# Kernel tuning notes

Measured on AMD Instinct MI355X. Metric: run time of the kernel, lower is better.

The kernel has to match this reference:

```python
import jax, jax.numpy as jnp
import numpy as np

B, S, E, H = 4, 2048, 1024, 16
D = E // H  # key_size


def setup_inputs() -> dict:
    key = jax.random.key(0)
    ks = jax.random.split(key, 6)
    s = 1.0 / np.sqrt(E)
    return {
        "X": jax.random.normal(ks[0], (B, S, E), dtype=jnp.float32),
        "Wq": jax.random.uniform(ks[1], (E, E), jnp.float32, -s, s),
        "Wk": jax.random.uniform(ks[2], (E, E), jnp.float32, -s, s),
        "Wv": jax.random.uniform(ks[3], (E, E), jnp.float32, -s, s),
        "Wo": jax.random.uniform(ks[4], (E, E), jnp.float32, -s, s),
        "bo": jax.random.uniform(ks[5], (E,), jnp.float32, -s, s),
    }


def reference(X, Wq, Wk, Wv, Wo, bo):
    # Linear layers: y = x @ W^T (torch convention), no bias for q/k/v
    def split(x):  # [B,S,E] -> [B,H,S,D]
        return x.reshape(B, S, H, D).transpose(0, 2, 1, 3)

    q = split(X @ Wq.T)
    k = split(X @ Wk.T)
    v = split(X @ Wv.T)
    scale = jnp.asarray(np.sqrt(D), dtype=X.dtype)
    scores = jnp.einsum("bhqd,bhkd->bhqk", q, k) / scale
    probs = jax.nn.softmax(scores, axis=-1)
    ctx = jnp.einsum("bhqk,bhkd->bhqd", probs, v)
    out = ctx.transpose(0, 2, 1, 3).reshape(B, S, E)
    return out @ Wo.T + bo
```

## Files before the change

### kernel.cpp

```cpp
#include <hip/hip_runtime.h>
#include <hip/hip_bf16.h>

typedef short bf16x8 __attribute__((ext_vector_type(8)));
typedef float f32x4  __attribute__((ext_vector_type(4)));

__device__ __forceinline__ short f2bf(float f) {
    union { float f; unsigned u; } x; x.f = f;
    unsigned r = x.u + 0x7fffu + ((x.u >> 16) & 1u);
    return (short)(r >> 16);
}

__device__ __forceinline__ unsigned rbits(float f) {
    union { float f; unsigned u; } x; x.f = f;
    return x.u + 0x8000u;
}
__device__ __forceinline__ int pack2(float a, float b) {
    return (int)__builtin_amdgcn_perm(rbits(b), rbits(a), 0x07060302u);
}

__device__ __forceinline__ f32x4 mfma32k(bf16x8 a, bf16x8 b, f32x4 c) {
    return __builtin_amdgcn_mfma_f32_16x16x32_bf16(a, b, c, 0, 0, 0);
}

#define GLDS16(g, l)                                                            \
    __builtin_amdgcn_global_load_lds(                                           \
        (const __attribute__((address_space(1))) void*)(g),                     \
        (__attribute__((address_space(3))) void*)(l), 16, 0, 0)

static constexpr int Bb = 4, Ss = 2048, Ee = 1024, Hh = 16, Dd = 64;
static constexpr int Mrows = Bb * Ss;
static constexpr float CL2 = 0.1803368801111204f;

__global__ void cvt_all(const float* __restrict__ X,  const float* __restrict__ Wq,
                        const float* __restrict__ Wk, const float* __restrict__ Wv,
                        const float* __restrict__ Wo,
                        short* __restrict__ Xb, short* __restrict__ Wqk,
                        short* __restrict__ Wvb, short* __restrict__ Wob) {
    int bid = blockIdx.x;
    const float* src; short* dst; int off; float scale = 1.0f;
    if (bid < 8192) {
        src = X; dst = Xb; off = bid * 1024;
    } else {
        int wsel = (bid - 8192) >> 10;
        off = ((bid - 8192) & 1023) * 1024;
        if      (wsel == 0) { src = Wq; dst = Wqk;                scale = CL2; }
        else if (wsel == 1) { src = Wk; dst = Wqk + Ee * Ee; }
        else if (wsel == 2) { src = Wv; dst = Wvb; }
        else                { src = Wo; dst = Wob; }
    }
    int i = off + threadIdx.x * 4;
    float4 v = *(const float4*)(src + i);
    short4 o;
    o.x = f2bf(v.x * scale); o.y = f2bf(v.y * scale);
    o.z = f2bf(v.z * scale); o.w = f2bf(v.w * scale);
    *(short4*)(dst + i) = o;
}

__global__ __launch_bounds__(256, 2)
void gemm_fused(const short* __restrict__ A0, const short* __restrict__ B0,
                short* __restrict__ C0,
                const short* __restrict__ A1, const short* __restrict__ B1,
                short* __restrict__ C1, int split) {
    __shared__ __align__(16) short sA[128 * 32];
    __shared__ __align__(16) short sB[128 * 32];
    const int t = threadIdx.x, w = t >> 6, l = t & 63;
    const int lane16 = l & 15, quad = l >> 4;
    const int wm = (w >> 1) * 64, wn = (w & 1) * 64;

    int bid = blockIdx.x;
    const short *A, *Bm; short* C;
    int bm, bn, ldc; bool perm;
    if (bid < split) {
        bm = bid & 63; bn = bid >> 6;
        A = A0; Bm = B0; C = C0; ldc = 2048; perm = false;
    } else {
        int id = bid - split;
        bm = id & 7; bn = id >> 3;
        A = A1; Bm = B1; C = C1; ldc = 8192; perm = true;
    }

    f32x4 acc[4][4] = {};
    const short* Ab  = A  + (size_t)bm * 128 * 1024;
    const short* Bbp = Bm + (size_t)bn * 128 * 1024;
    const int s0 = w * 64 + l;
    const int ldsOff = (w * 64) * 8;

    for (int k0 = 0; k0 < 1024; k0 += 32) {
#pragma unroll
        for (int p = 0; p < 2; ++p) {
            int s = p * 256 + s0;
            int row = s >> 2, cs = s & 3;
            GLDS16(Ab + (size_t)row * 1024 + k0 + cs * 8, sA + p * 2048 + ldsOff);
            GLDS16(Bbp + (size_t)row * 1024 + k0 + cs * 8, sB + p * 2048 + ldsOff);
        }
        __syncthreads();
        bf16x8 af[4], bfr[4];
#pragma unroll
        for (int i = 0; i < 4; ++i) {
            af[i]  = *(const bf16x8*)(sA + (wm + i * 16 + lane16) * 32 + quad * 8);
            bfr[i] = *(const bf16x8*)(sB + (wn + i * 16 + lane16) * 32 + quad * 8);
        }
#pragma unroll
        for (int i = 0; i < 4; ++i)
#pragma unroll
            for (int j = 0; j < 4; ++j)
                acc[i][j] = mfma32k(af[i], bfr[j], acc[i][j]);
        __syncthreads();
    }

    const int sEven = (lane16 >> 2) * 8 + (lane16 & 3);
#pragma unroll
    for (int i = 0; i < 4; ++i)
#pragma unroll
        for (int j = 0; j < 4; ++j) {
            int row = bm * 128 + wm + i * 16 + quad * 4;
            int col = bn * 128 + wn + j * 16 + lane16;
            if (perm) col = (col & ~31) | (sEven + (j & 1) * 4);
#pragma unroll
            for (int r = 0; r < 4; ++r)
                C[(size_t)(row + r) * ldc + col] = f2bf(acc[i][j][r]);
        }
}

__global__ __launch_bounds__(256, 2)
void gemm_out(const short* __restrict__ A, const short* __restrict__ Bm,
              float* __restrict__ C, const float* __restrict__ bias) {
    __shared__ __align__(16) short sA[128 * 32];
    __shared__ __align__(16) short sB[128 * 32];
    const int t = threadIdx.x, w = t >> 6, l = t & 63;
    const int lane16 = l & 15, quad = l >> 4;
    const int wm = (w >> 1) * 64, wn = (w & 1) * 64;
    const int bm = blockIdx.x, bn = blockIdx.y;

    f32x4 acc[4][4] = {};
    const short* Ab  = A  + (size_t)bm * 128 * 1024;
    const short* Bbp = Bm + (size_t)bn * 128 * 1024;
    const int s0 = w * 64 + l;
    const int ldsOff = (w * 64) * 8;

    for (int k0 = 0; k0 < 1024; k0 += 32) {
#pragma unroll
        for (int p = 0; p < 2; ++p) {
            int s = p * 256 + s0;
            int row = s >> 2, cs = s & 3;
            GLDS16(Ab + (size_t)row * 1024 + k0 + cs * 8, sA + p * 2048 + ldsOff);
            GLDS16(Bbp + (size_t)row * 1024 + k0 + cs * 8, sB + p * 2048 + ldsOff);
        }
        __syncthreads();
        bf16x8 af[4], bfr[4];
#pragma unroll
        for (int i = 0; i < 4; ++i) {
            af[i]  = *(const bf16x8*)(sA + (wm + i * 16 + lane16) * 32 + quad * 8);
            bfr[i] = *(const bf16x8*)(sB + (wn + i * 16 + lane16) * 32 + quad * 8);
        }
#pragma unroll
        for (int i = 0; i < 4; ++i)
#pragma unroll
            for (int j = 0; j < 4; ++j)
                acc[i][j] = mfma32k(af[i], bfr[j], acc[i][j]);
        __syncthreads();
    }

#pragma unroll
    for (int i = 0; i < 4; ++i)
#pragma unroll
        for (int j = 0; j < 4; ++j) {
            int row = bm * 128 + wm + i * 16 + quad * 4;
            int col = bn * 128 + wn + j * 16 + lane16;
            float bv = bias[col];
#pragma unroll
            for (int r = 0; r < 4; ++r)
                C[(size_t)(row + r) * 1024 + col] = acc[i][j][r] + bv;
        }
}

__global__ __launch_bounds__(256, 4)
void attn_kernel(const short* __restrict__ QK, const short* __restrict__ VT,
                 short* __restrict__ CTX) {
    __shared__ __align__(16) short sK[8192];
    __shared__ __align__(16) short sV[8192];
    const int t = threadIdx.x, w = t >> 6, l = t & 63;
    const int lane16 = l & 15, quad = l >> 4;
    const int bh = blockIdx.x, qt = blockIdx.y;
    const int b = bh >> 4, h = bh & 15;

    const int qx8 = (quad ^ ((lane16 >> 1) & 3)) * 8;

    const short* Qb = QK + ((size_t)(b * 2048 + qt * 128)) * 2048 + h * 64;
    const short* Vb = VT + ((size_t)(h * 64)) * 8192 + (size_t)b * 2048;
    const int ldsOff = (w * 64) * 8;

    int off_kq[4], off_v[4];
#pragma unroll
    for (int p = 0; p < 4; ++p) {
        int c = p * 256 + t;
        int sw = ((c & 3) ^ ((c >> 3) & 3)) * 8;
        off_kq[p] = ((c >> 2) & 127) * 2048 + (c >> 9) * 32 + sw;
        off_v[p]  = ((c >> 2) & 63) * 8192 + (c >> 8) * 32 + sw;
    }

#pragma unroll
    for (int p = 0; p < 4; ++p)
        GLDS16(Qb + off_kq[p], sK + p * 2048 + ldsOff);
    __syncthreads();
    bf16x8 qf[2][2];
#pragma unroll
    for (int mt = 0; mt < 2; ++mt)
#pragma unroll
        for (int ks = 0; ks < 2; ++ks)
            qf[mt][ks] = *(const bf16x8*)(sK + ks * 4096 + (w * 32 + mt * 16 + lane16) * 32 + qx8);
    __syncthreads();

    const short one = (short)0x3F80;
    const bf16x8 ONE8 = {one, one, one, one, one, one, one, one};
    f32x4 lacc[2] = {};
    f32x4 o[2][4] = {};

    const short* kptr = QK + ((size_t)(b * 2048)) * 2048 + 1024 + h * 64;
    const short* vptr = Vb;

    for (int kt = 0; kt < 16; ++kt) {
#pragma unroll
        for (int p = 0; p < 4; ++p)
            GLDS16(kptr + off_kq[p], sK + p * 2048 + ldsOff);
#pragma unroll
        for (int p = 0; p < 4; ++p)
            GLDS16(vptr + off_v[p], sV + p * 2048 + ldsOff);
        kptr += (size_t)128 * 2048;
        vptr += 128;
        __syncthreads();

#pragma unroll
        for (int a = 0; a < 4; ++a) {
            f32x4 sc[2][2] = {};
#pragma unroll
            for (int sub = 0; sub < 2; ++sub) {
                int nt = a * 2 + sub;
                bf16x8 kf0 = *(const bf16x8*)(sK + (nt * 16 + lane16) * 32 + qx8);
                bf16x8 kf1 = *(const bf16x8*)(sK + 4096 + (nt * 16 + lane16) * 32 + qx8);
#pragma unroll
                for (int mt = 0; mt < 2; ++mt) {
                    sc[mt][sub] = mfma32k(kf0, qf[mt][0], sc[mt][sub]);
                    sc[mt][sub] = mfma32k(kf1, qf[mt][1], sc[mt][sub]);
                }
            }
            bf16x8 pf[2];
#pragma unroll
            for (int mt = 0; mt < 2; ++mt) {
                union { int i[4]; bf16x8 v; } u;
#pragma unroll
                for (int sub = 0; sub < 2; ++sub) {
                    f32x4 e;
#pragma unroll
                    for (int r = 0; r < 4; ++r)
                        e[r] = __builtin_amdgcn_exp2f(sc[mt][sub][r]);
                    u.i[sub * 2]     = pack2(e[0], e[1]);
                    u.i[sub * 2 + 1] = pack2(e[2], e[3]);
                }
                pf[mt] = u.v;
            }
#pragma unroll
            for (int mt = 0; mt < 2; ++mt)
                lacc[mt] = mfma32k(pf[mt], ONE8, lacc[mt]);
#pragma unroll
            for (int dt = 0; dt < 4; ++dt) {
                bf16x8 vf = *(const bf16x8*)(sV + a * 2048 + (dt * 16 + lane16) * 32 + qx8);
#pragma unroll
                for (int mt = 0; mt < 2; ++mt)
                    o[mt][dt] = mfma32k(pf[mt], vf, o[mt][dt]);
            }
        }
        __syncthreads();
    }

#pragma unroll
    for (int mt = 0; mt < 2; ++mt)
#pragma unroll
        for (int r = 0; r < 4; ++r) {
            float inv = 1.0f / lacc[mt][r];
            int row = b * 2048 + qt * 128 + w * 32 + mt * 16 + quad * 4 + r;
#pragma unroll
            for (int dt = 0; dt < 4; ++dt)
                CTX[(size_t)row * 1024 + h * 64 + dt * 16 + lane16] = f2bf(o[mt][dt][r] * inv);
        }
}

extern "C" void kernel_launch(void* const* d_in, const int* in_sizes, int n_in,
                              void* d_out, int out_size, void* d_ws, size_t ws_size,
                              hipStream_t stream) {
    const float* X  = (const float*)d_in[0];
    const float* Wq = (const float*)d_in[1];
    const float* Wk = (const float*)d_in[2];
    const float* Wv = (const float*)d_in[3];
    const float* Wo = (const float*)d_in[4];
    const float* bo = (const float*)d_in[5];
    float* out = (float*)d_out;

    char* ws = (char*)d_ws;
    constexpr size_t OFF_XB  = 0;
    constexpr size_t OFF_WQK = OFF_XB  + (size_t)Mrows * Ee * 2;
    constexpr size_t OFF_WV  = OFF_WQK + (size_t)2 * Ee * Ee * 2;
    constexpr size_t OFF_WO  = OFF_WV  + (size_t)Ee * Ee * 2;
    constexpr size_t OFF_QK  = OFF_WO  + (size_t)Ee * Ee * 2;
    constexpr size_t OFF_VT  = OFF_QK  + (size_t)Mrows * 2048 * 2;
    constexpr size_t OFF_CTX = OFF_VT  + (size_t)Ee * Mrows * 2;
    short* Xb   = (short*)(ws + OFF_XB);
    short* Wqk  = (short*)(ws + OFF_WQK);
    short* Wvb  = (short*)(ws + OFF_WV);
    short* Wob  = (short*)(ws + OFF_WO);
    short* QKb  = (short*)(ws + OFF_QK);
    short* VTb  = (short*)(ws + OFF_VT);
    short* CTX  = (short*)(ws + OFF_CTX);

    cvt_all<<<12288, 256, 0, stream>>>(X, Wq, Wk, Wv, Wo, Xb, Wqk, Wvb, Wob);

    gemm_fused<<<1536, 256, 0, stream>>>(Xb, Wqk, QKb, Wvb, Xb, VTb, 1024);

    attn_kernel<<<dim3(Bb * Hh, Ss / 128), 256, 0, stream>>>(QKb, VTb, CTX);

    gemm_out<<<dim3(Mrows / 128, Ee / 128), 256, 0, stream>>>(CTX, Wob, out, bo);
}
```

Measured before the change: 259.5 us.

## Double-buffer K/V tiles in LDS with 64-key tiles to overlap loads

```diff
diff --git a/kernel.cpp b/kernel.cpp
--- a/kernel.cpp
+++ b/kernel.cpp
@@ -190,18 +190,22 @@
     const short* Vb = VT + ((size_t)(h * 64)) * 8192 + (size_t)b * 2048;
     const int ldsOff = (w * 64) * 8;
 
-    int off_kq[4], off_v[4];
+    int off_k[2], off_v[2];
+#pragma unroll
+    for (int p = 0; p < 2; ++p) {
+        int c = p * 256 + t;
+        int sw = ((c & 3) ^ ((c >> 3) & 3)) * 8;
+        off_k[p] = ((c >> 2) & 63) * 2048 + (c >> 8) * 32 + sw;
+        off_v[p] = ((c >> 2) & 63) * 8192 + (c >> 8) * 32 + sw;
+    }
+
 #pragma unroll
     for (int p = 0; p < 4; ++p) {
         int c = p * 256 + t;
         int sw = ((c & 3) ^ ((c >> 3) & 3)) * 8;
-        off_kq[p] = ((c >> 2) & 127) * 2048 + (c >> 9) * 32 + sw;
-        off_v[p]  = ((c >> 2) & 63) * 8192 + (c >> 8) * 32 + sw;
-    }
-
-#pragma unroll
-    for (int p = 0; p < 4; ++p)
-        GLDS16(Qb + off_kq[p], sK + p * 2048 + ldsOff);
+        GLDS16(Qb + ((c >> 2) & 127) * 2048 + (c >> 9) * 32 + sw,
+               sK + p * 2048 + ldsOff);
+    }
     __syncthreads();
     bf16x8 qf[2][2];
 #pragma unroll
@@ -219,25 +223,37 @@
     const short* kptr = QK + ((size_t)(b * 2048)) * 2048 + 1024 + h * 64;
     const short* vptr = Vb;
 
-    for (int kt = 0; kt < 16; ++kt) {
-#pragma unroll
-        for (int p = 0; p < 4; ++p)
-            GLDS16(kptr + off_kq[p], sK + p * 2048 + ldsOff);
-#pragma unroll
-        for (int p = 0; p < 4; ++p)
-            GLDS16(vptr + off_v[p], sV + p * 2048 + ldsOff);
-        kptr += (size_t)128 * 2048;
-        vptr += 128;
-        __syncthreads();
-
-#pragma unroll
-        for (int a = 0; a < 4; ++a) {
+#pragma unroll
+    for (int p = 0; p < 2; ++p) {
+        GLDS16(kptr + off_k[p], sK + p * 2048 + ldsOff);
+        GLDS16(vptr + off_v[p], sV + p * 2048 + ldsOff);
+    }
+    __syncthreads();
+
+    const short* kS = kptr + (size_t)64 * 2048;
+    const short* vS = vptr + 64;
+    int cur = 0;
+
+    for (int it = 0; it < 32; ++it) {
+        if (it < 31) {
+            int nxt = cur ^ 4096;
+#pragma unroll
+            for (int p = 0; p < 2; ++p) {
+                GLDS16(kS + off_k[p], sK + nxt + p * 2048 + ldsOff);
+                GLDS16(vS + off_v[p], sV + nxt + p * 2048 + ldsOff);
+            }
+            kS += (size_t)64 * 2048;
+            vS += 64;
+        }
+
+#pragma unroll
+        for (int a = 0; a < 2; ++a) {
             f32x4 sc[2][2] = {};
 #pragma unroll
             for (int sub = 0; sub < 2; ++sub) {
                 int nt = a * 2 + sub;
-                bf16x8 kf0 = *(const bf16x8*)(sK + (nt * 16 + lane16) * 32 + qx8);
-                bf16x8 kf1 = *(const bf16x8*)(sK + 4096 + (nt * 16 + lane16) * 32 + qx8);
+                bf16x8 kf0 = *(const bf16x8*)(sK + cur + (nt * 16 + lane16) * 32 + qx8);
+                bf16x8 kf1 = *(const bf16x8*)(sK + cur + 2048 + (nt * 16 + lane16) * 32 + qx8);
 #pragma unroll
                 for (int mt = 0; mt < 2; ++mt) {
                     sc[mt][sub] = mfma32k(kf0, qf[mt][0], sc[mt][sub]);
@@ -264,13 +280,14 @@
                 lacc[mt] = mfma32k(pf[mt], ONE8, lacc[mt]);
 #pragma unroll
             for (int dt = 0; dt < 4; ++dt) {
-                bf16x8 vf = *(const bf16x8*)(sV + a * 2048 + (dt * 16 + lane16) * 32 + qx8);
+                bf16x8 vf = *(const bf16x8*)(sV + cur + a * 2048 + (dt * 16 + lane16) * 32 + qx8);
 #pragma unroll
                 for (int mt = 0; mt < 2; ++mt)
                     o[mt][dt] = mfma32k(pf[mt], vf, o[mt][dt]);
             }
         }
         __syncthreads();
+        cur ^= 4096;
     }
 
 #pragma unroll
```

After: 258.8 us. Within noise of the previous version (-0.3%).
